# Performance work log

Hardware: AMD Instinct MI355X
Metric: run time of the kernel (lower is better)

Reference implementation:

```python
import jax, jax.numpy as jnp
import numpy as np

N_NODES = 50000
N_EDGES = 600000
IN_F = 128
HID = 128
OUT = 128
CLS = 128
N_GRAPHS = 64
LN_EPS = 1e-5


def _ln(h, g, b):
    m = jnp.mean(h, axis=-1, keepdims=True)
    v = jnp.var(h, axis=-1, keepdims=True)
    return (h - m) * jax.lax.rsqrt(v + LN_EPS) * g + b


def _segment_softmax(logits, seg, num_segments):
    m = jax.ops.segment_max(logits, seg, num_segments=num_segments)
    e = jnp.exp(logits - m[seg])
    s = jax.ops.segment_sum(e, seg, num_segments=num_segments)
    return e / s[seg]


def _gat_conv(x, src, dst, aux, w_lin, b_lin, aw1, ab1, lng, lnb, aw2, ab2):
    xl = x @ w_lin + b_lin                      # [N, out]
    sf = xl[src]                                # [E, out]
    df = xl[dst]                                # [E, out]
    ef = jnp.concatenate([sf, df, aux], axis=-1)  # [E, 2*out+2]
    h = jax.nn.relu(_ln(ef @ aw1 + ab1, lng, lnb))
    logits = h @ aw2 + ab2                      # [E, 1]
    att = _segment_softmax(logits, dst, xl.shape[0])
    num = jax.ops.segment_sum(sf * att, dst, num_segments=xl.shape[0])
    cnt = jax.ops.segment_sum(jnp.ones((src.shape[0], 1), xl.dtype), dst, num_segments=xl.shape[0])
    out = num / jnp.maximum(cnt, 1.0)           # scatter_mean (empty rows -> 0)
    return out + xl


def setup_inputs() -> dict:
    key = jax.random.key(0)
    ks = jax.random.split(key, 24)
    s = 0.05
    d = {
        'x': jax.random.normal(ks[0], (N_NODES, IN_F), jnp.float32),
        'edge_index': jax.random.randint(ks[1], (2, N_EDGES), 0, N_NODES, jnp.int64),
        'aux_info': jax.random.normal(ks[2], (N_EDGES, 2), jnp.float32),
        'batch': jnp.sort(jax.random.randint(ks[3], (N_NODES,), 0, N_GRAPHS, jnp.int64)),
        # conv1 params (in->hid)
        'w_lin1': jax.random.normal(ks[4], (IN_F, HID), jnp.float32) * s,
        'b_lin1': jnp.zeros((HID,), jnp.float32),
        'aw1_1': jax.random.normal(ks[5], (2 * HID + 2, HID), jnp.float32) * s,
        'ab1_1': jnp.zeros((HID,), jnp.float32),
        'lng1': jnp.ones((HID,), jnp.float32),
        'lnb1': jnp.zeros((HID,), jnp.float32),
        'aw2_1': jax.random.normal(ks[6], (HID, 1), jnp.float32) * s,
        'ab2_1': jnp.zeros((1,), jnp.float32),
        # conv2 params (hid->out)
        'w_lin2': jax.random.normal(ks[7], (HID, OUT), jnp.float32) * s,
        'b_lin2': jnp.zeros((OUT,), jnp.float32),
        'aw1_2': jax.random.normal(ks[8], (2 * OUT + 2, HID), jnp.float32) * s,
        'ab1_2': jnp.zeros((HID,), jnp.float32),
        'lng2': jnp.ones((HID,), jnp.float32),
        'lnb2': jnp.zeros((HID,), jnp.float32),
        'aw2_2': jax.random.normal(ks[9], (HID, 1), jnp.float32) * s,
        'ab2_2': jnp.zeros((1,), jnp.float32),
        # head
        'cls_w': jax.random.normal(ks[10], (OUT, CLS), jnp.float32) * s,
        'cls_b': jnp.zeros((CLS,), jnp.float32),
        'norm_g': jnp.ones((OUT,), jnp.float32),
        'norm_b': jnp.zeros((OUT,), jnp.float32),
    }
    return d


def reference(x, edge_index, aux_info, batch,
              w_lin1, b_lin1, aw1_1, ab1_1, lng1, lnb1, aw2_1, ab2_1,
              w_lin2, b_lin2, aw1_2, ab1_2, lng2, lnb2, aw2_2, ab2_2,
              cls_w, cls_b, norm_g, norm_b):
    src, dst = edge_index[0], edge_index[1]
    h = _gat_conv(x, src, dst, aux_info, w_lin1, b_lin1, aw1_1, ab1_1, lng1, lnb1, aw2_1, ab2_1)
    h = jax.nn.relu(h)
    h = _gat_conv(h, src, dst, aux_info, w_lin2, b_lin2, aw1_2, ab1_2, lng2, lnb2, aw2_2, ab2_2)
    h = _ln(h, norm_g, norm_b)                  # [N, out]
    fusion = jax.ops.segment_max(h, batch, num_segments=N_GRAPHS)  # global max pool
    cls = fusion @ cls_w + cls_b                # [G, cls]
    return (h, cls)
```

## Files before the change

kernel.cpp:

```cpp
#include <hip/hip_runtime.h>
#include <math.h>

typedef __attribute__((ext_vector_type(8))) short short8v;
typedef __attribute__((ext_vector_type(4))) float f32x4;
typedef __attribute__((ext_vector_type(2))) float f32x2;

__device__ __forceinline__ unsigned short f2bf(float f) {
    union { float f; unsigned int u; } v; v.f = f;
    unsigned int r = v.u + 0x7FFFu + ((v.u >> 16) & 1u);
    return (unsigned short)(r >> 16);
}
__device__ __forceinline__ float bflo(unsigned int v) {
    union { unsigned int u; float f; } x; x.u = v << 16; return x.f;
}
__device__ __forceinline__ float bfhi(unsigned int v) {
    union { unsigned int u; float f; } x; x.u = v & 0xFFFF0000u; return x.f;
}
__device__ __forceinline__ unsigned char f2fp8(float f) {
    return (unsigned char)(__builtin_amdgcn_cvt_pk_fp8_f32(f, f, 0, false) & 0xFF);
}
__device__ __forceinline__ unsigned pkrtz(float a, float b) {
    unsigned d;
    asm("v_cvt_pkrtz_f16_f32 %0, %1, %2" : "=v"(d) : "v"(a), "v"(b));
    return d;
}
__device__ __forceinline__ float fdot2a(unsigned a, unsigned b, float c) {
    float d;
    asm("v_dot2_f32_f16 %0, %1, %2, %3" : "=v"(d) : "v"(a), "v"(b), "v"(c));
    return d;
}
__device__ __forceinline__ unsigned pk_fma_f16(unsigned a, unsigned b, unsigned c) {
    unsigned d;
    asm("v_pk_fma_f16 %0, %1, %2, %3" : "=v"(d) : "v"(a), "v"(b), "v"(c));
    return d;
}
__device__ __forceinline__ unsigned pk_max0_f16(unsigned a, unsigned z) {
    unsigned d;
    asm("v_pk_max_f16 %0, %1, %2" : "=v"(d) : "v"(a), "v"(z));
    return d;
}

__global__ __launch_bounds__(256) void prep_kernel(const float* __restrict__ s0,
                                                   const float* __restrict__ s1,
                                                   const float* __restrict__ s2,
                                                   const float* __restrict__ s3,
                                                   const float* __restrict__ s4,
                                                   const float* __restrict__ s5,
                                                   unsigned short* __restrict__ Wp,
                                                   const int* __restrict__ dst,
                                                   int* __restrict__ deg, int E) {
    int b = blockIdx.x;
    if (b < 384) {
        int which = b >> 6;
        const float* W = (which == 0) ? s0 : (which == 1) ? s1 : (which == 2) ? s2
                       : (which == 3) ? s3 : (which == 4) ? s4 : s5;
        int t = (b & 63) * 256 + threadIdx.x;
        int j = t & 7, l = (t >> 3) & 63, ct = (t >> 9) & 7, ks = t >> 12;
        int k = ks * 32 + (l >> 4) * 8 + j;
        int n = ct * 16 + (l & 15);
        Wp[which * 16384 + t] = f2bf(W[k * 128 + n]);
    } else {
        int e = (b - 384) * 256 + threadIdx.x;
        if (e < E) atomicAdd(&deg[dst[e]], 1);
    }
}

__global__ __launch_bounds__(256) void scan1_kernel(const int* __restrict__ deg,
                                                    int* __restrict__ rp,
                                                    int* __restrict__ bsum, int N) {
    const int lane = threadIdx.x & 63, wid = threadIdx.x >> 6;
    int i = blockIdx.x * 256 + threadIdx.x;
    int v = (i < N) ? deg[i] : 0;
    int val = v;
#pragma unroll
    for (int off = 1; off < 64; off <<= 1) {
        int t = __shfl_up(val, off, 64);
        if (lane >= off) val += t;
    }
    __shared__ int ws[4];
    if (lane == 63) ws[wid] = val;
    __syncthreads();
    int pre = 0;
#pragma unroll
    for (int w = 0; w < 4; ++w) pre += (w < wid) ? ws[w] : 0;
    int incl = pre + val;
    if (i < N) rp[i] = incl - v;
    if (threadIdx.x == 255) bsum[blockIdx.x] = incl;
}

__global__ __launch_bounds__(256) void scan23_kernel(int* __restrict__ rp,
                                                     const int* __restrict__ bsum,
                                                     const int* __restrict__ batch,
                                                     int* __restrict__ gstart,
                                                     int* __restrict__ gend,
                                                     int N, int E) {
    const int lane = threadIdx.x & 63, wid = threadIdx.x >> 6;
    const int b = blockIdx.x;
    int v = ((int)threadIdx.x < b) ? bsum[threadIdx.x] : 0;
#pragma unroll
    for (int m = 32; m >= 1; m >>= 1) v += __shfl_xor(v, m, 64);
    __shared__ int ws[4];
    if (lane == 0) ws[wid] = v;
    __syncthreads();
    int offset = ws[0] + ws[1] + ws[2] + ws[3];
    int i = b * 256 + threadIdx.x;
    if (i < N) {
        rp[i] += offset;
        int bb = batch[i];
        if (i == 0 || batch[i - 1] != bb) gstart[bb] = i;
        if (i == N - 1 || batch[i + 1] != bb) gend[bb] = i + 1;
    }
    if (b == 0 && threadIdx.x == 0) rp[N] = E;
}

__global__ __launch_bounds__(256) void linpq_scat_kernel(
    const float* __restrict__ Av,
    const unsigned short* __restrict__ WpL, const float* __restrict__ bias,
    const unsigned short* __restrict__ WpP, const unsigned short* __restrict__ WpQ,
    const float* __restrict__ ab1,
    unsigned short* __restrict__ Dbf, unsigned char* __restrict__ Vf8,
    unsigned char* __restrict__ Pf8, unsigned char* __restrict__ Qf8, int M, int LB,
    const int* __restrict__ src, const int* __restrict__ dst,
    const float* __restrict__ aux, const int* __restrict__ rowptr,
    int* __restrict__ cursor, uint2* __restrict__ er, int E) {
    __shared__ unsigned short lds[32][136];
    __shared__ unsigned char ldsV[32][128];
    __shared__ unsigned char ldsP[32][128];
    __shared__ unsigned char ldsQ[32][128];

    const int b = blockIdx.x;
    int bi;
    bool isScat;
    if (b < 2 * LB) { isScat = ((b & 1) == 0); bi = b >> 1; }
    else            { isScat = true;           bi = LB + (b - 2 * LB); }

    if (isScat) {
        int e = bi * 256 + (int)threadIdx.x;
        if (e < E) {
            int d = dst[e];
            int pos = rowptr[d] + atomicAdd(&cursor[d], 1);
            float2 a = *(const float2*)(aux + 2 * e);
            uint2 r;
            r.x = (unsigned)src[e] | ((unsigned)d << 16);
            r.y = (unsigned)f2bf(a.x) | ((unsigned)f2bf(a.y) << 16);
            er[pos] = r;
        }
        return;
    }

    const int l = threadIdx.x & 63, w = threadIdx.x >> 6;
    const int tile = w >> 1, ch = w & 1;
    const int rowb = bi * 32;
    const int rowbase = rowb + tile * 16;
    const int r = rowbase + (l & 15);
    const int kc = (l >> 4) * 8;

    short8v afr[4];
    if (r < M) {
        const float* ap = Av + (size_t)r * 128 + kc;
#pragma unroll
        for (int ks = 0; ks < 4; ++ks) {
            float4 x0 = *(const float4*)(ap + ks * 32);
            float4 x1 = *(const float4*)(ap + ks * 32 + 4);
            unsigned short u[8] = {f2bf(x0.x), f2bf(x0.y), f2bf(x0.z), f2bf(x0.w),
                                   f2bf(x1.x), f2bf(x1.y), f2bf(x1.z), f2bf(x1.w)};
            afr[ks] = *(short8v*)u;
        }
    } else {
#pragma unroll
        for (int ks = 0; ks < 4; ++ks)
#pragma unroll
            for (int j = 0; j < 8; ++j) afr[ks][j] = 0;
    }

    f32x4 acc[4];
#pragma unroll
    for (int c = 0; c < 4; ++c)
#pragma unroll
        for (int j = 0; j < 4; ++j) acc[c][j] = 0.f;

    const short8v* wl = (const short8v*)WpL;
#pragma unroll
    for (int ks = 0; ks < 4; ++ks)
#pragma unroll
        for (int c = 0; c < 4; ++c)
            acc[c] = __builtin_amdgcn_mfma_f32_16x16x32_bf16(
                afr[ks], wl[(ks * 8 + ch * 4 + c) * 64 + l], acc[c], 0, 0, 0);

    const int lrb = tile * 16 + (l >> 4) * 4;
#pragma unroll
    for (int c = 0; c < 4; ++c) {
        int col = (ch * 4 + c) * 16 + (l & 15);
        float bv = bias[col];
#pragma unroll
        for (int j = 0; j < 4; ++j) {
            float v = acc[c][j] + bv;
            lds[lrb + j][col] = f2bf(v);
            ldsV[lrb + j][col] = f2fp8(v);
        }
    }
    __syncthreads();

    {
        int r2 = threadIdx.x >> 3, q2 = threadIdx.x & 7;
        if (rowb + r2 < M) {
            *(uint4*)(Dbf + (size_t)(rowb + r2) * 128 + q2 * 16) =
                *(uint4*)&lds[r2][q2 * 16];
            *(uint4*)(Dbf + (size_t)(rowb + r2) * 128 + q2 * 16 + 8) =
                *(uint4*)&lds[r2][q2 * 16 + 8];
            *(uint4*)(Vf8 + (size_t)(rowb + r2) * 128 + q2 * 16) =
                *(uint4*)&ldsV[r2][q2 * 16];
        }
    }

    short8v xfr[4];
#pragma unroll
    for (int ks = 0; ks < 4; ++ks)
        xfr[ks] = *(const short8v*)&lds[tile * 16 + (l & 15)][kc + ks * 32];

    f32x4 accP[4], accQ[4];
#pragma unroll
    for (int c = 0; c < 4; ++c)
#pragma unroll
        for (int j = 0; j < 4; ++j) { accP[c][j] = 0.f; accQ[c][j] = 0.f; }

    const short8v* wp = (const short8v*)WpP;
    const short8v* wq = (const short8v*)WpQ;
#pragma unroll
    for (int ks = 0; ks < 4; ++ks)
#pragma unroll
        for (int c = 0; c < 4; ++c) {
            accP[c] = __builtin_amdgcn_mfma_f32_16x16x32_bf16(
                xfr[ks], wp[(ks * 8 + ch * 4 + c) * 64 + l], accP[c], 0, 0, 0);
            accQ[c] = __builtin_amdgcn_mfma_f32_16x16x32_bf16(
                xfr[ks], wq[(ks * 8 + ch * 4 + c) * 64 + l], accQ[c], 0, 0, 0);
        }

#pragma unroll
    for (int c = 0; c < 4; ++c) {
        int col = (ch * 4 + c) * 16 + (l & 15);
        float b1v = ab1[col];
#pragma unroll
        for (int j = 0; j < 4; ++j) {
            ldsP[lrb + j][col] = f2fp8(accP[c][j]);
            ldsQ[lrb + j][col] = f2fp8(accQ[c][j] + b1v);
        }
    }
    __syncthreads();
    {
        int r2 = threadIdx.x >> 3, q2 = threadIdx.x & 7;
        if (rowb + r2 < M) {
            *(uint4*)(Pf8 + (size_t)(rowb + r2) * 128 + q2 * 16) =
                *(uint4*)&ldsP[r2][q2 * 16];
            *(uint4*)(Qf8 + (size_t)(rowb + r2) * 128 + q2 * 16) =
                *(uint4*)&ldsQ[r2][q2 * 16];
        }
    }
}

__global__ __launch_bounds__(256) void linpq_kernel(const unsigned short* __restrict__ Av,
                                                    const unsigned short* __restrict__ WpL,
                                                    const float* __restrict__ bias,
                                                    const unsigned short* __restrict__ WpP,
                                                    const unsigned short* __restrict__ WpQ,
                                                    const float* __restrict__ ab1,
                                                    unsigned short* __restrict__ Dbf,
                                                    unsigned char* __restrict__ Vf8,
                                                    unsigned char* __restrict__ Pf8,
                                                    unsigned char* __restrict__ Qf8, int M) {
    __shared__ unsigned short lds[32][136];
    __shared__ unsigned char ldsV[32][128];
    __shared__ unsigned char ldsP[32][128];
    __shared__ unsigned char ldsQ[32][128];
    const int l = threadIdx.x & 63, w = threadIdx.x >> 6;
    const int tile = w >> 1, ch = w & 1;
    const int rowb = blockIdx.x * 32;
    const int rowbase = rowb + tile * 16;
    const int r = rowbase + (l & 15);
    const int kc = (l >> 4) * 8;

    short8v afr[4];
    if (r < M) {
        const unsigned short* ap = Av + (size_t)r * 128 + kc;
#pragma unroll
        for (int ks = 0; ks < 4; ++ks)
            afr[ks] = *(const short8v*)(ap + ks * 32);
    } else {
#pragma unroll
        for (int ks = 0; ks < 4; ++ks)
#pragma unroll
            for (int j = 0; j < 8; ++j) afr[ks][j] = 0;
    }

    f32x4 acc[4];
#pragma unroll
    for (int c = 0; c < 4; ++c)
#pragma unroll
        for (int j = 0; j < 4; ++j) acc[c][j] = 0.f;

    const short8v* wl = (const short8v*)WpL;
#pragma unroll
    for (int ks = 0; ks < 4; ++ks)
#pragma unroll
        for (int c = 0; c < 4; ++c)
            acc[c] = __builtin_amdgcn_mfma_f32_16x16x32_bf16(
                afr[ks], wl[(ks * 8 + ch * 4 + c) * 64 + l], acc[c], 0, 0, 0);

    const int lrb = tile * 16 + (l >> 4) * 4;
#pragma unroll
    for (int c = 0; c < 4; ++c) {
        int col = (ch * 4 + c) * 16 + (l & 15);
        float bv = bias[col];
#pragma unroll
        for (int j = 0; j < 4; ++j) {
            float v = acc[c][j] + bv;
            lds[lrb + j][col] = f2bf(v);
            ldsV[lrb + j][col] = f2fp8(v);
        }
    }
    __syncthreads();

    {
        int r2 = threadIdx.x >> 3, q2 = threadIdx.x & 7;
        if (rowb + r2 < M) {
            *(uint4*)(Dbf + (size_t)(rowb + r2) * 128 + q2 * 16) =
                *(uint4*)&lds[r2][q2 * 16];
            *(uint4*)(Dbf + (size_t)(rowb + r2) * 128 + q2 * 16 + 8) =
                *(uint4*)&lds[r2][q2 * 16 + 8];
            *(uint4*)(Vf8 + (size_t)(rowb + r2) * 128 + q2 * 16) =
                *(uint4*)&ldsV[r2][q2 * 16];
        }
    }

    short8v xfr[4];
#pragma unroll
    for (int ks = 0; ks < 4; ++ks)
        xfr[ks] = *(const short8v*)&lds[tile * 16 + (l & 15)][kc + ks * 32];

    f32x4 accP[4], accQ[4];
#pragma unroll
    for (int c = 0; c < 4; ++c)
#pragma unroll
        for (int j = 0; j < 4; ++j) { accP[c][j] = 0.f; accQ[c][j] = 0.f; }

    const short8v* wp = (const short8v*)WpP;
    const short8v* wq = (const short8v*)WpQ;
#pragma unroll
    for (int ks = 0; ks < 4; ++ks)
#pragma unroll
        for (int c = 0; c < 4; ++c) {
            accP[c] = __builtin_amdgcn_mfma_f32_16x16x32_bf16(
                xfr[ks], wp[(ks * 8 + ch * 4 + c) * 64 + l], accP[c], 0, 0, 0);
            accQ[c] = __builtin_amdgcn_mfma_f32_16x16x32_bf16(
                xfr[ks], wq[(ks * 8 + ch * 4 + c) * 64 + l], accQ[c], 0, 0, 0);
        }

#pragma unroll
    for (int c = 0; c < 4; ++c) {
        int col = (ch * 4 + c) * 16 + (l & 15);
        float b1v = ab1[col];
#pragma unroll
        for (int j = 0; j < 4; ++j) {
            ldsP[lrb + j][col] = f2fp8(accP[c][j]);
            ldsQ[lrb + j][col] = f2fp8(accQ[c][j] + b1v);
        }
    }
    __syncthreads();
    {
        int r2 = threadIdx.x >> 3, q2 = threadIdx.x & 7;
        if (rowb + r2 < M) {
            *(uint4*)(Pf8 + (size_t)(rowb + r2) * 128 + q2 * 16) =
                *(uint4*)&ldsP[r2][q2 * 16];
            *(uint4*)(Qf8 + (size_t)(rowb + r2) * 128 + q2 * 16) =
                *(uint4*)&ldsQ[r2][q2 * 16];
        }
    }
}

__global__ __launch_bounds__(256, 4) void attn_edge_kernel(
    const unsigned char* __restrict__ Pf8, const unsigned char* __restrict__ Qf8,
    const uint2* __restrict__ er,
    const float* __restrict__ wa0, const float* __restrict__ wa1,
    const float* __restrict__ lng, const float* __restrict__ lnb,
    const float* __restrict__ aw2, const float* __restrict__ ab2,
    float* __restrict__ wt, int E) {
    __shared__ float lwf[256];
    __shared__ unsigned lwh[192];
    {
        int idx = threadIdx.x;
        int arr = idx >> 7, rem = idx & 127;
        int par = rem >> 6, c = (rem >> 2) & 15, e = rem & 3;
        const float* sp = arr ? wa1 : wa0;
        lwf[(((arr * 16 + c) << 1) + par) * 4 + e] = sp[rem];
        if (idx < 192) {
            int a2 = idx >> 6, rem2 = idx & 63;
            int p2 = rem2 >> 5;
            int c2 = (rem2 >> 1) & 15;
            int pr = rem2 & 1;
            int chn = p2 * 64 + c2 * 4 + pr * 2;
            const float* s2 = (a2 == 0) ? lng : (a2 == 1) ? lnb : aw2;
            lwh[(((a2 * 16 + c2) << 1) + p2) * 2 + pr] = pkrtz(s2[chn], s2[chn + 1]);
        }
    }
    __syncthreads();
    const int slot = blockIdx.x * 128 + ((int)threadIdx.x >> 1);
    if (slot >= E) return;
    const int par = threadIdx.x & 1;
    const unsigned one2 = 0x3C003C00u;
    const unsigned zero2 = 0u;
    const int co = par << 6;

    uint2 ev = er[slot];
    const int sn = (int)(ev.x & 0xFFFFu);
    const int dn = (int)(ev.x >> 16);
    const float ax = bflo(ev.y), ay = bfhi(ev.y);

    const uint4* prow = (const uint4*)(Pf8 + (size_t)sn * 128 + co);
    const uint4* qrow = (const uint4*)(Qf8 + (size_t)dn * 128 + co);

    float r1 = 0.f, r2 = 0.f;
    unsigned tp[32];

#pragma unroll
    for (int g = 0; g < 4; ++g) {
        uint4 pv = prow[g];
        uint4 qv = qrow[g];
        unsigned pwa[4] = {pv.x, pv.y, pv.z, pv.w};
        unsigned qwa[4] = {qv.x, qv.y, qv.z, qv.w};
#pragma unroll
        for (int cc = 0; cc < 4; ++cc) {
            const int c = g * 4 + cc;
            f32x2 plo = __builtin_amdgcn_cvt_pk_f32_fp8((int)pwa[cc], false);
            f32x2 phi = __builtin_amdgcn_cvt_pk_f32_fp8((int)pwa[cc], true);
            f32x2 qlo = __builtin_amdgcn_cvt_pk_f32_fp8((int)qwa[cc], false);
            f32x2 qhi = __builtin_amdgcn_cvt_pk_f32_fp8((int)qwa[cc], true);
            float4 w0v = *(const float4*)&lwf[((c << 1) + par) * 4];
            float4 w1v = *(const float4*)&lwf[(((16 + c) << 1) + par) * 4];
            float t0 = plo[0] + qlo[0] + ax * w0v.x + ay * w1v.x;
            float t1 = plo[1] + qlo[1] + ax * w0v.y + ay * w1v.y;
            float t2 = phi[0] + qhi[0] + ax * w0v.z + ay * w1v.z;
            float t3 = phi[1] + qhi[1] + ax * w0v.w + ay * w1v.w;
            unsigned p0 = pkrtz(t0, t1);
            unsigned p1 = pkrtz(t2, t3);
            tp[2 * c] = p0;
            tp[2 * c + 1] = p1;
            r1 = fdot2a(p0, one2, r1);
            r1 = fdot2a(p1, one2, r1);
            r2 = fdot2a(p0, p0, r2);
            r2 = fdot2a(p1, p1, r2);
        }
    }
    r1 += __shfl_xor(r1, 1, 64);
    r2 += __shfl_xor(r2, 1, 64);
    float mean = r1 * (1.f / 128.f);
    float rstd = rsqrtf(r2 * (1.f / 128.f) - mean * mean + 1e-5f);
    float mr = mean * rstd;
    unsigned rstd2 = pkrtz(rstd, rstd);
    unsigned nmr2 = pkrtz(-mr, -mr);

    float dot = 0.f;
#pragma unroll
    for (int c = 0; c < 16; ++c) {
        unsigned base = (unsigned)(((c << 1) + par) * 2);
        uint2 gg = *(const uint2*)&lwh[base];
        uint2 ll = *(const uint2*)&lwh[64 + base];
        uint2 ww = *(const uint2*)&lwh[128 + base];
        unsigned u0 = pk_fma_f16(tp[2 * c], rstd2, nmr2);
        u0 = pk_fma_f16(u0, gg.x, ll.x);
        u0 = pk_max0_f16(u0, zero2);
        dot = fdot2a(u0, ww.x, dot);
        unsigned u1 = pk_fma_f16(tp[2 * c + 1], rstd2, nmr2);
        u1 = pk_fma_f16(u1, gg.y, ll.y);
        u1 = pk_max0_f16(u1, zero2);
        dot = fdot2a(u1, ww.y, dot);
    }
    dot += __shfl_xor(dot, 1, 64);
    if (par == 0) wt[slot] = __expf(dot + ab2[0]);
}

template <int MODE>
__global__ __launch_bounds__(256) void aggr_kernel(
    const unsigned short* __restrict__ xlbf, const unsigned char* __restrict__ Vf8,
    const float* __restrict__ wt,
    const uint2* __restrict__ er, const int* __restrict__ rowptr,
    const float* __restrict__ g, const float* __restrict__ b,
    void* __restrict__ out, int N) {
    const int lane8 = threadIdx.x & 7;
    const int v = blockIdx.x * 32 + ((int)threadIdx.x >> 3);
    if (v >= N) return;
    const int jb = lane8 * 16;

    const int s0 = rowptr[v], s1e = rowptr[v + 1];
    const int deg = s1e - s0;
    float acc[16];
#pragma unroll
    for (int k = 0; k < 16; ++k) acc[k] = 0.f;
    float wsum = 0.f;

    uint4 v0 = make_uint4(0, 0, 0, 0), v1 = v0;
    float wb0 = 0.f, wb1 = 0.f;
#define GATH2(idx, VV, WW)                                                       \
    if ((idx) < s1e) {                                                           \
        int sn_ = (int)(er[idx].x & 0xFFFFu);                                    \
        VV = *(const uint4*)(Vf8 + (size_t)sn_ * 128 + jb);                      \
        WW = wt[idx];                                                            \
    }
    GATH2(s0, v0, wb0)
    GATH2(s0 + 1, v1, wb1)

    for (int i = s0; i < s1e; i += 2) {
        uint4 c0 = v0, c1 = v1;
        float u0 = wb0;
        float u1 = (i + 1 < s1e) ? wb1 : 0.f;
        GATH2(i + 2, v0, wb0)
        GATH2(i + 3, v1, wb1)
        wsum += u0 + u1;
        unsigned d0[4] = {c0.x, c0.y, c0.z, c0.w};
        unsigned d1[4] = {c1.x, c1.y, c1.z, c1.w};
#pragma unroll
        for (int k = 0; k < 4; ++k) {
            f32x2 alo = __builtin_amdgcn_cvt_pk_f32_fp8((int)d0[k], false);
            f32x2 ahi = __builtin_amdgcn_cvt_pk_f32_fp8((int)d0[k], true);
            f32x2 blo = __builtin_amdgcn_cvt_pk_f32_fp8((int)d1[k], false);
            f32x2 bhi = __builtin_amdgcn_cvt_pk_f32_fp8((int)d1[k], true);
            acc[4 * k + 0] += u0 * alo[0] + u1 * blo[0];
            acc[4 * k + 1] += u0 * alo[1] + u1 * blo[1];
            acc[4 * k + 2] += u0 * ahi[0] + u1 * bhi[0];
            acc[4 * k + 3] += u0 * ahi[1] + u1 * bhi[1];
        }
    }
#undef GATH2

    const float ns = (deg > 0) ? 1.f / (wsum * (float)deg) : 0.f;
    float o[16];
    const unsigned short* xp = xlbf + (size_t)v * 128 + jb;
    uint4 xa = *(const uint4*)xp;
    uint4 xb = *(const uint4*)(xp + 8);
    unsigned xw[8] = {xa.x, xa.y, xa.z, xa.w, xb.x, xb.y, xb.z, xb.w};
#pragma unroll
    for (int k = 0; k < 8; ++k) {
        o[2 * k] = bflo(xw[k]) + acc[2 * k] * ns;
        o[2 * k + 1] = bfhi(xw[k]) + acc[2 * k + 1] * ns;
    }

    if (MODE == 0) {
        unsigned short* op = (unsigned short*)out + (size_t)v * 128 + jb;
        unsigned opk[8];
#pragma unroll
        for (int k = 0; k < 8; ++k)
            opk[k] = (unsigned)f2bf(fmaxf(o[2 * k], 0.f)) |
                     ((unsigned)f2bf(fmaxf(o[2 * k + 1], 0.f)) << 16);
        *(uint4*)op = make_uint4(opk[0], opk[1], opk[2], opk[3]);
        *(uint4*)(op + 8) = make_uint4(opk[4], opk[5], opk[6], opk[7]);
    } else {
        float r1 = 0.f, r2 = 0.f;
#pragma unroll
        for (int k = 0; k < 16; ++k) { r1 += o[k]; r2 = fmaf(o[k], o[k], r2); }
#pragma unroll
        for (int mk = 4; mk >= 1; mk >>= 1) {
            r1 += __shfl_xor(r1, mk, 64);
            r2 += __shfl_xor(r2, mk, 64);
        }
        float mean = r1 * (1.f / 128.f);
        float rstd = rsqrtf(r2 * (1.f / 128.f) - mean * mean + 1e-5f);
        float mr = mean * rstd;
        float* op = (float*)out + (size_t)v * 128 + jb;
#pragma unroll
        for (int k4 = 0; k4 < 4; ++k4) {
            float4 gv = *(const float4*)(g + jb + 4 * k4);
            float4 bv = *(const float4*)(b + jb + 4 * k4);
            float4 r;
            r.x = fmaf(fmaf(o[4 * k4 + 0], rstd, -mr), gv.x, bv.x);
            r.y = fmaf(fmaf(o[4 * k4 + 1], rstd, -mr), gv.y, bv.y);
            r.z = fmaf(fmaf(o[4 * k4 + 2], rstd, -mr), gv.z, bv.z);
            r.w = fmaf(fmaf(o[4 * k4 + 3], rstd, -mr), gv.w, bv.w);
            *(float4*)(op + 4 * k4) = r;
        }
    }
}

__global__ __launch_bounds__(128) void pool1_kernel(const float* __restrict__ h,
                                                    const int* __restrict__ gstart,
                                                    const int* __restrict__ gend,
                                                    float* __restrict__ part) {
    int gph = blockIdx.x >> 4;
    int sl = blockIdx.x & 15;
    int col = threadIdx.x;
    int s = gstart[gph], e = gend[gph];
    float m = -INFINITY;
    for (int r = s + sl; r < e; r += 16) m = fmaxf(m, h[(size_t)r * 128 + col]);
    part[(size_t)blockIdx.x * 128 + col] = m;
}

__global__ __launch_bounds__(128) void cls_kernel(const float* __restrict__ part,
                                                  const float* __restrict__ cw,
                                                  const float* __restrict__ cb,
                                                  float* __restrict__ out) {
    int gph = blockIdx.x, c = threadIdx.x;
    float m = -INFINITY;
#pragma unroll
    for (int sl = 0; sl < 16; ++sl) m = fmaxf(m, part[(size_t)(gph * 16 + sl) * 128 + c]);
    __shared__ float f[128];
    f[c] = m;
    __syncthreads();
    float acc = cb[c];
#pragma unroll 8
    for (int k = 0; k < 128; ++k) acc += f[k] * cw[k * 128 + c];
    out[gph * 128 + c] = acc;
}

extern "C" void kernel_launch(void* const* d_in, const int* in_sizes, int n_in,
                              void* d_out, int out_size, void* d_ws, size_t ws_size,
                              hipStream_t stream) {
    const float* x      = (const float*)d_in[0];
    const int*   ei     = (const int*)d_in[1];
    const float* aux    = (const float*)d_in[2];
    const int*   batch  = (const int*)d_in[3];
    const float* w_lin1 = (const float*)d_in[4];
    const float* b_lin1 = (const float*)d_in[5];
    const float* aw1_1  = (const float*)d_in[6];
    const float* ab1_1  = (const float*)d_in[7];
    const float* lng1   = (const float*)d_in[8];
    const float* lnb1   = (const float*)d_in[9];
    const float* aw2_1  = (const float*)d_in[10];
    const float* ab2_1  = (const float*)d_in[11];
    const float* w_lin2 = (const float*)d_in[12];
    const float* b_lin2 = (const float*)d_in[13];
    const float* aw1_2  = (const float*)d_in[14];
    const float* ab1_2  = (const float*)d_in[15];
    const float* lng2   = (const float*)d_in[16];
    const float* lnb2   = (const float*)d_in[17];
    const float* aw2_2  = (const float*)d_in[18];
    const float* ab2_2  = (const float*)d_in[19];
    const float* cls_w  = (const float*)d_in[20];
    const float* cls_b  = (const float*)d_in[21];
    const float* norm_g = (const float*)d_in[22];
    const float* norm_b = (const float*)d_in[23];

    const int N = in_sizes[0] / 128;
    const int E = in_sizes[2] / 2;
    const int G = 64;
    const int* src = ei;
    const int* dst = ei + E;

    char* wsp = (char*)d_ws;
    unsigned short* xlbf  = (unsigned short*)wsp;   wsp += (size_t)N * 128 * 2;
    unsigned short* h1bf  = (unsigned short*)wsp;   wsp += (size_t)N * 128 * 2;
    unsigned char*  Pf8   = (unsigned char*)wsp;    wsp += (size_t)N * 128;
    unsigned char*  Qf8   = (unsigned char*)wsp;    wsp += (size_t)N * 128;
    unsigned char*  Vf8   = (unsigned char*)wsp;    wsp += (size_t)N * 128;
    unsigned short* wpack = (unsigned short*)wsp;   wsp += 6 * 16384 * 2;
    float*          part  = (float*)wsp;            wsp += (size_t)1024 * 128 * 4;
    uint2*          er    = (uint2*)wsp;            wsp += (size_t)E * 8;
    float*          wt    = (float*)wsp;            wsp += (size_t)E * 4;
    int*            bsum    = (int*)wsp;            wsp += 256 * 4;
    int*            deg     = (int*)wsp;            wsp += (size_t)N * 4;
    int*            cursor  = (int*)wsp;            wsp += (size_t)N * 4;
    int*            rowptr  = (int*)wsp;            wsp += (size_t)(N + 1) * 4;
    int*            gstart  = (int*)wsp;            wsp += (size_t)G * 4;
    int*            gend    = (int*)wsp;            wsp += (size_t)G * 4;

    unsigned short* wp_lin1 = wpack;
    unsigned short* wp_s1   = wpack + 16384;
    unsigned short* wp_d1   = wpack + 2 * 16384;
    unsigned short* wp_lin2 = wpack + 3 * 16384;
    unsigned short* wp_s2   = wpack + 4 * 16384;
    unsigned short* wp_d2   = wpack + 5 * 16384;

    float* hout   = (float*)d_out;
    float* clsout = hout + (size_t)N * 128;

    hipMemsetAsync(deg, 0, (size_t)(2 * N) * sizeof(int), stream);
    hipMemsetAsync(gstart, 0, (size_t)(2 * G) * sizeof(int), stream);

    const int eb = (E + 255) / 256;
    const int nb = (N + 255) / 256;
    const int lb = (N + 31) / 32;
    const int atb = (E + 127) / 128;
    const int agb = (N + 31) / 32;

    prep_kernel<<<384 + eb, 256, 0, stream>>>(w_lin1, aw1_1, aw1_1 + 128 * 128,
                                              w_lin2, aw1_2, aw1_2 + 128 * 128,
                                              wpack, dst, deg, E);
    scan1_kernel<<<nb, 256, 0, stream>>>(deg, rowptr, bsum, N);
    scan23_kernel<<<nb, 256, 0, stream>>>(rowptr, bsum, batch, gstart, gend, N, E);

    linpq_scat_kernel<<<lb + eb, 256, 0, stream>>>(x, wp_lin1, b_lin1, wp_s1, wp_d1,
                                                   ab1_1, xlbf, Vf8, Pf8, Qf8, N, lb,
                                                   src, dst, aux, rowptr, cursor, er, E);
    attn_edge_kernel<<<atb, 256, 0, stream>>>(Pf8, Qf8, er,
                                              aw1_1 + 256 * 128, aw1_1 + 257 * 128,
                                              lng1, lnb1, aw2_1, ab2_1, wt, E);
    aggr_kernel<0><<<agb, 256, 0, stream>>>(xlbf, Vf8, wt, er, rowptr,
                                            nullptr, nullptr, h1bf, N);
    linpq_kernel<<<lb, 256, 0, stream>>>(h1bf, wp_lin2, b_lin2, wp_s2, wp_d2, ab1_2,
                                         xlbf, Vf8, Pf8, Qf8, N);
    attn_edge_kernel<<<atb, 256, 0, stream>>>(Pf8, Qf8, er,
                                              aw1_2 + 256 * 128, aw1_2 + 257 * 128,
                                              lng2, lnb2, aw2_2, ab2_2, wt, E);
    aggr_kernel<1><<<agb, 256, 0, stream>>>(xlbf, Vf8, wt, er, rowptr,
                                            norm_g, norm_b, hout, N);
    pool1_kernel<<<G * 16, 128, 0, stream>>>(hout, gstart, gend, part);
    cls_kernel<<<G, 128, 0, stream>>>(part, cls_w, cls_b, clsout);
}
```

Before: 217.3 us.

## Fuse edge attention and neighbor aggregation into one per-node-block kernel

Merges the per-edge attention-weight kernel and the CSR aggregation kernel into a single kernel. Each block of 32 destination nodes computes the attention weights for its contiguous edge range in chunks of 128 into LDS, then aggregates from LDS. This removes the global weight buffer round-trip and one launch per conv layer. In exchange, the edge-compute phase is now load-balanced per node block rather than per edge, adds block-wide barriers per chunk, and drops the occupancy hint from the launch bounds.

```diff
diff --git a/kernel.cpp b/kernel.cpp
--- a/kernel.cpp
+++ b/kernel.cpp
@@ -377,163 +377,167 @@
     }
 }
 
-__global__ __launch_bounds__(256, 4) void attn_edge_kernel(
+template <int MODE>
+__global__ __launch_bounds__(256) void conv_fused_kernel(
     const unsigned char* __restrict__ Pf8, const unsigned char* __restrict__ Qf8,
-    const uint2* __restrict__ er,
+    const unsigned short* __restrict__ xlbf, const unsigned char* __restrict__ Vf8,
+    const uint2* __restrict__ er, const int* __restrict__ rowptr,
     const float* __restrict__ wa0, const float* __restrict__ wa1,
     const float* __restrict__ lng, const float* __restrict__ lnb,
     const float* __restrict__ aw2, const float* __restrict__ ab2,
-    float* __restrict__ wt, int E) {
+    const float* __restrict__ g, const float* __restrict__ b,
+    void* __restrict__ out, int N) {
     __shared__ float lwf[256];
     __shared__ unsigned lwh[192];
+    __shared__ float wt_lds[128];
     {
         int idx = threadIdx.x;
         int arr = idx >> 7, rem = idx & 127;
-        int par = rem >> 6, c = (rem >> 2) & 15, e = rem & 3;
+        int pr2 = rem >> 6, c = (rem >> 2) & 15, e = rem & 3;
         const float* sp = arr ? wa1 : wa0;
-        lwf[(((arr * 16 + c) << 1) + par) * 4 + e] = sp[rem];
+        lwf[(((arr * 16 + c) << 1) + pr2) * 4 + e] = sp[rem];
         if (idx < 192) {
             int a2 = idx >> 6, rem2 = idx & 63;
-            int p2 = rem2 >> 5;
-            int c2 = (rem2 >> 1) & 15;
-            int pr = rem2 & 1;
+            int p2 = rem2 >> 5, c2 = (rem2 >> 1) & 15, pr = rem2 & 1;
             int chn = p2 * 64 + c2 * 4 + pr * 2;
             const float* s2 = (a2 == 0) ? lng : (a2 == 1) ? lnb : aw2;
             lwh[(((a2 * 16 + c2) << 1) + p2) * 2 + pr] = pkrtz(s2[chn], s2[chn + 1]);
         }
     }
+
+    const int v0 = blockIdx.x * 32;
+    const int lane8 = threadIdx.x & 7;
+    const int vI = v0 + ((int)threadIdx.x >> 3);
+    const int jb = lane8 * 16;
+    int sv0 = 0, sv1 = 0;
+    if (vI < N) { sv0 = rowptr[vI]; sv1 = rowptr[vI + 1]; }
+    const int s0 = rowptr[v0];
+    const int s1 = rowptr[(v0 + 32 < N) ? (v0 + 32) : N];
     __syncthreads();
-    const int slot = blockIdx.x * 128 + ((int)threadIdx.x >> 1);
-    if (slot >= E) return;
+
     const int par = threadIdx.x & 1;
-    const unsigned one2 = 0x3C003C00u;
-    const unsigned zero2 = 0u;
+    const unsigned one2 = 0x3C003C00u, zero2 = 0u;
     const int co = par << 6;
-
-    uint2 ev = er[slot];
-    const int sn = (int)(ev.x & 0xFFFFu);
-    const int dn = (int)(ev.x >> 16);
-    const float ax = bflo(ev.y), ay = bfhi(ev.y);
-
-    const uint4* prow = (const uint4*)(Pf8 + (size_t)sn * 128 + co);
-    const uint4* qrow = (const uint4*)(Qf8 + (size_t)dn * 128 + co);
-
-    float r1 = 0.f, r2 = 0.f;
-    unsigned tp[32];
-
-#pragma unroll
-    for (int g = 0; g < 4; ++g) {
-        uint4 pv = prow[g];
-        uint4 qv = qrow[g];
-        unsigned pwa[4] = {pv.x, pv.y, pv.z, pv.w};
-        unsigned qwa[4] = {qv.x, qv.y, qv.z, qv.w};
-#pragma unroll
-        for (int cc = 0; cc < 4; ++cc) {
-            const int c = g * 4 + cc;
-            f32x2 plo = __builtin_amdgcn_cvt_pk_f32_fp8((int)pwa[cc], false);
-            f32x2 phi = __builtin_amdgcn_cvt_pk_f32_fp8((int)pwa[cc], true);
-            f32x2 qlo = __builtin_amdgcn_cvt_pk_f32_fp8((int)qwa[cc], false);
-            f32x2 qhi = __builtin_amdgcn_cvt_pk_f32_fp8((int)qwa[cc], true);
-            float4 w0v = *(const float4*)&lwf[((c << 1) + par) * 4];
-            float4 w1v = *(const float4*)&lwf[(((16 + c) << 1) + par) * 4];
-            float t0 = plo[0] + qlo[0] + ax * w0v.x + ay * w1v.x;
-            float t1 = plo[1] + qlo[1] + ax * w0v.y + ay * w1v.y;
-            float t2 = phi[0] + qhi[0] + ax * w0v.z + ay * w1v.z;
-            float t3 = phi[1] + qhi[1] + ax * w0v.w + ay * w1v.w;
-            unsigned p0 = pkrtz(t0, t1);
-            unsigned p1 = pkrtz(t2, t3);
-            tp[2 * c] = p0;
-            tp[2 * c + 1] = p1;
-            r1 = fdot2a(p0, one2, r1);
-            r1 = fdot2a(p1, one2, r1);
-            r2 = fdot2a(p0, p0, r2);
-            r2 = fdot2a(p1, p1, r2);
-        }
-    }
-    r1 += __shfl_xor(r1, 1, 64);
-    r2 += __shfl_xor(r2, 1, 64);
-    float mean = r1 * (1.f / 128.f);
-    float rstd = rsqrtf(r2 * (1.f / 128.f) - mean * mean + 1e-5f);
-    float mr = mean * rstd;
-    unsigned rstd2 = pkrtz(rstd, rstd);
-    unsigned nmr2 = pkrtz(-mr, -mr);
-
-    float dot = 0.f;
-#pragma unroll
-    for (int c = 0; c < 16; ++c) {
-        unsigned base = (unsigned)(((c << 1) + par) * 2);
-        uint2 gg = *(const uint2*)&lwh[base];
-        uint2 ll = *(const uint2*)&lwh[64 + base];
-        uint2 ww = *(const uint2*)&lwh[128 + base];
-        unsigned u0 = pk_fma_f16(tp[2 * c], rstd2, nmr2);
-        u0 = pk_fma_f16(u0, gg.x, ll.x);
-        u0 = pk_max0_f16(u0, zero2);
-        dot = fdot2a(u0, ww.x, dot);
-        unsigned u1 = pk_fma_f16(tp[2 * c + 1], rstd2, nmr2);
-        u1 = pk_fma_f16(u1, gg.y, ll.y);
-        u1 = pk_max0_f16(u1, zero2);
-        dot = fdot2a(u1, ww.y, dot);
-    }
-    dot += __shfl_xor(dot, 1, 64);
-    if (par == 0) wt[slot] = __expf(dot + ab2[0]);
-}
-
-template <int MODE>
-__global__ __launch_bounds__(256) void aggr_kernel(
-    const unsigned short* __restrict__ xlbf, const unsigned char* __restrict__ Vf8,
-    const float* __restrict__ wt,
-    const uint2* __restrict__ er, const int* __restrict__ rowptr,
-    const float* __restrict__ g, const float* __restrict__ b,
-    void* __restrict__ out, int N) {
-    const int lane8 = threadIdx.x & 7;
-    const int v = blockIdx.x * 32 + ((int)threadIdx.x >> 3);
-    if (v >= N) return;
-    const int jb = lane8 * 16;
-
-    const int s0 = rowptr[v], s1e = rowptr[v + 1];
-    const int deg = s1e - s0;
+    const float ab2v = ab2[0];
+
     float acc[16];
 #pragma unroll
     for (int k = 0; k < 16; ++k) acc[k] = 0.f;
     float wsum = 0.f;
 
-    uint4 v0 = make_uint4(0, 0, 0, 0), v1 = v0;
-    float wb0 = 0.f, wb1 = 0.f;
-#define GATH2(idx, VV, WW)                                                       \
-    if ((idx) < s1e) {                                                           \
-        int sn_ = (int)(er[idx].x & 0xFFFFu);                                    \
-        VV = *(const uint4*)(Vf8 + (size_t)sn_ * 128 + jb);                      \
-        WW = wt[idx];                                                            \
-    }
-    GATH2(s0, v0, wb0)
-    GATH2(s0 + 1, v1, wb1)
-
-    for (int i = s0; i < s1e; i += 2) {
-        uint4 c0 = v0, c1 = v1;
-        float u0 = wb0;
-        float u1 = (i + 1 < s1e) ? wb1 : 0.f;
-        GATH2(i + 2, v0, wb0)
-        GATH2(i + 3, v1, wb1)
-        wsum += u0 + u1;
-        unsigned d0[4] = {c0.x, c0.y, c0.z, c0.w};
-        unsigned d1[4] = {c1.x, c1.y, c1.z, c1.w};
-#pragma unroll
-        for (int k = 0; k < 4; ++k) {
-            f32x2 alo = __builtin_amdgcn_cvt_pk_f32_fp8((int)d0[k], false);
-            f32x2 ahi = __builtin_amdgcn_cvt_pk_f32_fp8((int)d0[k], true);
-            f32x2 blo = __builtin_amdgcn_cvt_pk_f32_fp8((int)d1[k], false);
-            f32x2 bhi = __builtin_amdgcn_cvt_pk_f32_fp8((int)d1[k], true);
-            acc[4 * k + 0] += u0 * alo[0] + u1 * blo[0];
-            acc[4 * k + 1] += u0 * alo[1] + u1 * blo[1];
-            acc[4 * k + 2] += u0 * ahi[0] + u1 * bhi[0];
-            acc[4 * k + 3] += u0 * ahi[1] + u1 * bhi[1];
-        }
-    }
-#undef GATH2
-
+    for (int chunk = s0; chunk < s1; chunk += 128) {
+        const int slot = chunk + ((int)threadIdx.x >> 1);
+        if (slot < s1) {
+            uint2 ev = er[slot];
+            const int sn = (int)(ev.x & 0xFFFFu);
+            const int dn = (int)(ev.x >> 16);
+            const float ax = bflo(ev.y), ay = bfhi(ev.y);
+            const uint4* prow = (const uint4*)(Pf8 + (size_t)sn * 128 + co);
+            const uint4* qrow = (const uint4*)(Qf8 + (size_t)dn * 128 + co);
+            float r1 = 0.f, r2 = 0.f;
+            unsigned tp[32];
+#pragma unroll
+            for (int gq = 0; gq < 4; ++gq) {
+                uint4 pv = prow[gq];
+                uint4 qv = qrow[gq];
+                unsigned pwa[4] = {pv.x, pv.y, pv.z, pv.w};
+                unsigned qwa[4] = {qv.x, qv.y, qv.z, qv.w};
+#pragma unroll
+                for (int cc = 0; cc < 4; ++cc) {
+                    const int c = gq * 4 + cc;
+                    f32x2 plo = __builtin_amdgcn_cvt_pk_f32_fp8((int)pwa[cc], false);
+                    f32x2 phi = __builtin_amdgcn_cvt_pk_f32_fp8((int)pwa[cc], true);
+                    f32x2 qlo = __builtin_amdgcn_cvt_pk_f32_fp8((int)qwa[cc], false);
+                    f32x2 qhi = __builtin_amdgcn_cvt_pk_f32_fp8((int)qwa[cc], true);
+                    float4 w0v = *(const float4*)&lwf[((c << 1) + par) * 4];
+                    float4 w1v = *(const float4*)&lwf[(((16 + c) << 1) + par) * 4];
+                    float t0 = plo[0] + qlo[0] + ax * w0v.x + ay * w1v.x;
+                    float t1 = plo[1] + qlo[1] + ax * w0v.y + ay * w1v.y;
+                    float t2 = phi[0] + qhi[0] + ax * w0v.z + ay * w1v.z;
+                    float t3 = phi[1] + qhi[1] + ax * w0v.w + ay * w1v.w;
+                    unsigned p0 = pkrtz(t0, t1);
+                    unsigned p1 = pkrtz(t2, t3);
+                    tp[2 * c] = p0;
+                    tp[2 * c + 1] = p1;
+                    r1 = fdot2a(p0, one2, r1);
+                    r1 = fdot2a(p1, one2, r1);
+                    r2 = fdot2a(p0, p0, r2);
+                    r2 = fdot2a(p1, p1, r2);
+                }
+            }
+            r1 += __shfl_xor(r1, 1, 64);
+            r2 += __shfl_xor(r2, 1, 64);
+            float mean = r1 * (1.f / 128.f);
+            float rstd = rsqrtf(r2 * (1.f / 128.f) - mean * mean + 1e-5f);
+            float mr = mean * rstd;
+            unsigned rstd2 = pkrtz(rstd, rstd);
+            unsigned nmr2 = pkrtz(-mr, -mr);
+            float dot = 0.f;
+#pragma unroll
+            for (int c = 0; c < 16; ++c) {
+                unsigned base = (unsigned)(((c << 1) + par) * 2);
+                uint2 gg = *(const uint2*)&lwh[base];
+                uint2 ll = *(const uint2*)&lwh[64 + base];
+                uint2 ww = *(const uint2*)&lwh[128 + base];
+                unsigned u0 = pk_fma_f16(tp[2 * c], rstd2, nmr2);
+                u0 = pk_fma_f16(u0, gg.x, ll.x);
+                u0 = pk_max0_f16(u0, zero2);
+                dot = fdot2a(u0, ww.x, dot);
+                unsigned u1 = pk_fma_f16(tp[2 * c + 1], rstd2, nmr2);
+                u1 = pk_fma_f16(u1, gg.y, ll.y);
+                u1 = pk_max0_f16(u1, zero2);
+                dot = fdot2a(u1, ww.y, dot);
+            }
+            dot += __shfl_xor(dot, 1, 64);
+            if (par == 0) wt_lds[(int)threadIdx.x >> 1] = __expf(dot + ab2v);
+        }
+        __syncthreads();
+
+        const int chunkEnd = (chunk + 128 < s1) ? (chunk + 128) : s1;
+        int lo = (sv0 > chunk) ? sv0 : chunk;
+        int hi = (sv1 < chunkEnd) ? sv1 : chunkEnd;
+        uint4 pv0 = make_uint4(0, 0, 0, 0), pv1 = pv0;
+        float w0 = 0.f, w1 = 0.f;
+#define GATHF(idx, VV, WW)                                                       \
+        if ((idx) < hi) {                                                        \
+            int sn_ = (int)(er[idx].x & 0xFFFFu);                                \
+            VV = *(const uint4*)(Vf8 + (size_t)sn_ * 128 + jb);                  \
+            WW = wt_lds[(idx) - chunk];                                          \
+        }
+        if (lo < hi) {
+            GATHF(lo, pv0, w0)
+            GATHF(lo + 1, pv1, w1)
+            for (int i = lo; i < hi; i += 2) {
+                uint4 c0 = pv0, c1 = pv1;
+                float u0 = w0;
+                float u1 = (i + 1 < hi) ? w1 : 0.f;
+                GATHF(i + 2, pv0, w0)
+                GATHF(i + 3, pv1, w1)
+                wsum += u0 + u1;
+                unsigned d0[4] = {c0.x, c0.y, c0.z, c0.w};
+                unsigned d1[4] = {c1.x, c1.y, c1.z, c1.w};
+#pragma unroll
+                for (int k = 0; k < 4; ++k) {
+                    f32x2 alo = __builtin_amdgcn_cvt_pk_f32_fp8((int)d0[k], false);
+                    f32x2 ahi = __builtin_amdgcn_cvt_pk_f32_fp8((int)d0[k], true);
+                    f32x2 blo = __builtin_amdgcn_cvt_pk_f32_fp8((int)d1[k], false);
+                    f32x2 bhi = __builtin_amdgcn_cvt_pk_f32_fp8((int)d1[k], true);
+                    acc[4 * k + 0] += u0 * alo[0] + u1 * blo[0];
+                    acc[4 * k + 1] += u0 * alo[1] + u1 * blo[1];
+                    acc[4 * k + 2] += u0 * ahi[0] + u1 * bhi[0];
+                    acc[4 * k + 3] += u0 * ahi[1] + u1 * bhi[1];
+                }
+            }
+        }
+#undef GATHF
+        __syncthreads();
+    }
+
+    if (vI >= N) return;
+    const int deg = sv1 - sv0;
     const float ns = (deg > 0) ? 1.f / (wsum * (float)deg) : 0.f;
     float o[16];
-    const unsigned short* xp = xlbf + (size_t)v * 128 + jb;
+    const unsigned short* xp = xlbf + (size_t)vI * 128 + jb;
     uint4 xa = *(const uint4*)xp;
     uint4 xb = *(const uint4*)(xp + 8);
     unsigned xw[8] = {xa.x, xa.y, xa.z, xa.w, xb.x, xb.y, xb.z, xb.w};
@@ -544,7 +548,7 @@
     }
 
     if (MODE == 0) {
-        unsigned short* op = (unsigned short*)out + (size_t)v * 128 + jb;
+        unsigned short* op = (unsigned short*)out + (size_t)vI * 128 + jb;
         unsigned opk[8];
 #pragma unroll
         for (int k = 0; k < 8; ++k)
@@ -564,17 +568,17 @@
         float mean = r1 * (1.f / 128.f);
         float rstd = rsqrtf(r2 * (1.f / 128.f) - mean * mean + 1e-5f);
         float mr = mean * rstd;
-        float* op = (float*)out + (size_t)v * 128 + jb;
+        float* op = (float*)out + (size_t)vI * 128 + jb;
 #pragma unroll
         for (int k4 = 0; k4 < 4; ++k4) {
             float4 gv = *(const float4*)(g + jb + 4 * k4);
             float4 bv = *(const float4*)(b + jb + 4 * k4);
-            float4 r;
-            r.x = fmaf(fmaf(o[4 * k4 + 0], rstd, -mr), gv.x, bv.x);
-            r.y = fmaf(fmaf(o[4 * k4 + 1], rstd, -mr), gv.y, bv.y);
-            r.z = fmaf(fmaf(o[4 * k4 + 2], rstd, -mr), gv.z, bv.z);
-            r.w = fmaf(fmaf(o[4 * k4 + 3], rstd, -mr), gv.w, bv.w);
-            *(float4*)(op + 4 * k4) = r;
+            float4 rr;
+            rr.x = fmaf(fmaf(o[4 * k4 + 0], rstd, -mr), gv.x, bv.x);
+            rr.y = fmaf(fmaf(o[4 * k4 + 1], rstd, -mr), gv.y, bv.y);
+            rr.z = fmaf(fmaf(o[4 * k4 + 2], rstd, -mr), gv.z, bv.z);
+            rr.w = fmaf(fmaf(o[4 * k4 + 3], rstd, -mr), gv.w, bv.w);
+            *(float4*)(op + 4 * k4) = rr;
         }
     }
 }
@@ -652,7 +656,6 @@
     unsigned short* wpack = (unsigned short*)wsp;   wsp += 6 * 16384 * 2;
     float*          part  = (float*)wsp;            wsp += (size_t)1024 * 128 * 4;
     uint2*          er    = (uint2*)wsp;            wsp += (size_t)E * 8;
-    float*          wt    = (float*)wsp;            wsp += (size_t)E * 4;
     int*            bsum    = (int*)wsp;            wsp += 256 * 4;
     int*            deg     = (int*)wsp;            wsp += (size_t)N * 4;
     int*            cursor  = (int*)wsp;            wsp += (size_t)N * 4;
@@ -676,8 +679,7 @@
     const int eb = (E + 255) / 256;
     const int nb = (N + 255) / 256;
     const int lb = (N + 31) / 32;
-    const int atb = (E + 127) / 128;
-    const int agb = (N + 31) / 32;
+    const int cfb = (N + 31) / 32;
 
     prep_kernel<<<384 + eb, 256, 0, stream>>>(w_lin1, aw1_1, aw1_1 + 128 * 128,
                                               w_lin2, aw1_2, aw1_2 + 128 * 128,
@@ -688,18 +690,16 @@
     linpq_scat_kernel<<<lb + eb, 256, 0, stream>>>(x, wp_lin1, b_lin1, wp_s1, wp_d1,
                                                    ab1_1, xlbf, Vf8, Pf8, Qf8, N, lb,
                                                    src, dst, aux, rowptr, cursor, er, E);
-    attn_edge_kernel<<<atb, 256, 0, stream>>>(Pf8, Qf8, er,
-                                              aw1_1 + 256 * 128, aw1_1 + 257 * 128,
-                                              lng1, lnb1, aw2_1, ab2_1, wt, E);
-    aggr_kernel<0><<<agb, 256, 0, stream>>>(xlbf, Vf8, wt, er, rowptr,
-                                            nullptr, nullptr, h1bf, N);
+    conv_fused_kernel<0><<<cfb, 256, 0, stream>>>(Pf8, Qf8, xlbf, Vf8, er, rowptr,
+                                                  aw1_1 + 256 * 128, aw1_1 + 257 * 128,
+                                                  lng1, lnb1, aw2_1, ab2_1,
+                                                  nullptr, nullptr, h1bf, N);
     linpq_kernel<<<lb, 256, 0, stream>>>(h1bf, wp_lin2, b_lin2, wp_s2, wp_d2, ab1_2,
                                          xlbf, Vf8, Pf8, Qf8, N);
-    attn_edge_kernel<<<atb, 256, 0, stream>>>(Pf8, Qf8, er,
-                                              aw1_2 + 256 * 128, aw1_2 + 257 * 128,
-                                              lng2, lnb2, aw2_2, ab2_2, wt, E);
-    aggr_kernel<1><<<agb, 256, 0, stream>>>(xlbf, Vf8, wt, er, rowptr,
-                                            norm_g, norm_b, hout, N);
+    conv_fused_kernel<1><<<cfb, 256, 0, stream>>>(Pf8, Qf8, xlbf, Vf8, er, rowptr,
+                                                  aw1_2 + 256 * 128, aw1_2 + 257 * 128,
+                                                  lng2, lnb2, aw2_2, ab2_2,
+                                                  norm_g, norm_b, hout, N);
     pool1_kernel<<<G * 16, 128, 0, stream>>>(hout, gstart, gend, part);
     cls_kernel<<<G, 128, 0, stream>>>(part, cls_w, cls_b, clsout);
 }
```

After: 307.2 us. 1.41x slower.
